# Kernel optimization log

Hardware: AMD Instinct MI355X
Metric: run time of the kernel (lower is better)

## Reference

```python
import jax, jax.numpy as jnp
import numpy as np

D_MODEL = 1024
EXPERT_SIZE = 512
N_EXPERTS = 8
GROUP_SIZE = 32
BATCH = 32
SEQ = 2048
TEMPERATURE = 1.0


def setup_inputs() -> dict:
    key = jax.random.key(0)
    k_x, k_l1, k_l2, k_c = jax.random.split(key, 4)
    x = jax.random.normal(k_x, (BATCH, SEQ, D_MODEL), dtype=jnp.float32)
    # truncated-normal-style init approximated with normal scaled by 1/sqrt(fan_in)
    lin1 = jax.random.normal(k_l1, (N_EXPERTS, D_MODEL, EXPERT_SIZE), dtype=jnp.float32) * (D_MODEL ** -0.5)
    lin2 = jax.random.normal(k_l2, (N_EXPERTS, EXPERT_SIZE, D_MODEL), dtype=jnp.float32) * (EXPERT_SIZE ** -0.5)
    controller = jax.random.normal(k_c, (D_MODEL, N_EXPERTS), dtype=jnp.float32) * (D_MODEL ** -0.5)
    return {"x": x, "lin1": lin1, "lin2": lin2, "controller": controller}


def reference(x, lin1, lin2, controller):
    B, S, D = x.shape
    # group_tokens: sparsity_dim=0 -> transpose to (S, B, D), split batch into groups
    xg = jnp.transpose(x, (1, 0, 2)).reshape(S, B // GROUP_SIZE, GROUP_SIZE, D)  # (s, g, k, d)
    # controller logits, softmax over the group (token) axis k (dim=-2)
    logits = jnp.einsum("sgkd,de->sgke", xg, controller) / TEMPERATURE
    merge_w = jax.nn.softmax(logits, axis=-2)  # (s, g, k, e)
    emit_w = merge_w  # default: emit softmax over tokens, same temp -> reuse
    # merge: weighted sum of tokens per expert
    merged = jnp.einsum("sgke,sgkd->sged", merge_w, xg)  # (s, g, e, d)
    # per-expert MLP
    h = jax.nn.relu(jnp.einsum("sged,edf->sgef", merged, lin1))  # (s, g, e, f)
    expert_out = jnp.einsum("sgef,efd->sged", h, lin2)  # (s, g, e, d)
    # emit back to tokens
    out = jnp.einsum("sgke,sged->sgkd", emit_w, expert_out)  # (s, g, k, d)
    # redistribute: (S, B, D) -> (B, S, D)
    return jnp.transpose(out.reshape(S, B, D), (1, 0, 2))
```

## Files before the change

### kernel.cpp

```cpp
#include <hip/hip_runtime.h>
#include <hip/hip_bf16.h>

#define SS 2048
#define BB 32
#define DD 1024
#define FF 512
#define EE 8

typedef __attribute__((ext_vector_type(8))) short short8;
typedef __attribute__((ext_vector_type(8))) unsigned short ushort8v;
typedef __attribute__((ext_vector_type(4))) unsigned short ushort4v;
typedef __attribute__((ext_vector_type(4))) float f32x4;

__device__ inline unsigned short f2bf(float f) {
  union { float f; unsigned u; } v; v.f = f;
  return (unsigned short)((v.u + 0x7FFFu + ((v.u >> 16) & 1u)) >> 16);
}
__device__ inline float bf2f(unsigned short h) {
  union { unsigned u; float f; } v; v.u = ((unsigned)h) << 16;
  return v.f;
}

__global__ __launch_bounds__(256) void transpose_bf16(
    const float* __restrict__ in, unsigned short* __restrict__ out, int K, int N) {
  __shared__ float tile[32][33];
  int e = blockIdx.z;
  const float* inp = in + (size_t)e * K * N;
  unsigned short* outp = out + (size_t)e * K * N;
  int k0 = blockIdx.x * 32, n0 = blockIdx.y * 32;
  int tx = threadIdx.x;
  int ty = threadIdx.y;
#pragma unroll
  for (int i = 0; i < 4; i++) {
    int k = ty + i * 8;
    tile[k][tx] = inp[(size_t)(k0 + k) * N + n0 + tx];
  }
  __syncthreads();
#pragma unroll
  for (int i = 0; i < 4; i++) {
    int n = ty + i * 8;
    outp[(size_t)(n0 + n) * K + k0 + tx] = f2bf(tile[tx][n]);
  }
}

__global__ __launch_bounds__(256) void logits_k(
    const float* __restrict__ x,
    const float* __restrict__ ctrl,
    float* __restrict__ lgT) {
  int t = threadIdx.x;
  __shared__ __align__(16) float cs[EE * DD];
  for (int i = t; i < DD * EE; i += 256) {
    int d = i >> 3, e = i & 7;
    cs[e * DD + (d ^ (((d >> 6) & 7) << 2))] = ctrl[i];
  }
  __syncthreads();

  int g = t >> 4, c = t & 15;
  int m0 = blockIdx.x * 64 + g * 4;
  const float* xr = x + (size_t)m0 * DD;
  float acc[4][8] = {};
#pragma unroll 4
  for (int i = 0; i < 16; i++) {
    int db = c * 4 + i * 64;
    float4 c4[8];
#pragma unroll
    for (int e = 0; e < 8; e++)
      c4[e] = *(const float4*)&cs[e * DD + i * 64 + ((c ^ (i & 7)) << 2)];
#pragma unroll
    for (int r = 0; r < 4; r++) {
      float4 xv = *(const float4*)&xr[(size_t)r * DD + db];
#pragma unroll
      for (int e = 0; e < 8; e++)
        acc[r][e] += xv.x * c4[e].x + xv.y * c4[e].y + xv.z * c4[e].z + xv.w * c4[e].w;
    }
  }
#pragma unroll
  for (int off = 1; off < 16; off <<= 1)
#pragma unroll
    for (int r = 0; r < 4; r++)
#pragma unroll
      for (int e = 0; e < 8; e++)
        acc[r][e] += __shfl_xor(acc[r][e], off, 64);
  if (c == 0) {
#pragma unroll
    for (int r = 0; r < 4; r++) {
      int m = m0 + r;
      int s = m & (SS - 1), k = m >> 11;
      float* p = &lgT[((size_t)s * BB + k) * EE];
      float4 lo = {acc[r][0], acc[r][1], acc[r][2], acc[r][3]};
      float4 hi = {acc[r][4], acc[r][5], acc[r][6], acc[r][7]};
      *(float4*)p = lo;
      *(float4*)(p + 4) = hi;
    }
  }
}

__global__ __launch_bounds__(256) void softmax_k(
    const float* __restrict__ lgT,
    float* __restrict__ mw) {
  int t = threadIdx.x;
  int sl = t >> 5, k = t & 31;
  size_t s = (size_t)blockIdx.x * 8 + sl;
  const float* p = &lgT[(s * BB + k) * EE];
  float v[8];
  float4 lo = *(const float4*)p, hi = *(const float4*)(p + 4);
  v[0]=lo.x; v[1]=lo.y; v[2]=lo.z; v[3]=lo.w; v[4]=hi.x; v[5]=hi.y; v[6]=hi.z; v[7]=hi.w;
  float mx[8];
#pragma unroll
  for (int e = 0; e < 8; e++) mx[e] = v[e];
#pragma unroll
  for (int off = 1; off < 32; off <<= 1)
#pragma unroll
    for (int e = 0; e < 8; e++)
      mx[e] = fmaxf(mx[e], __shfl_xor(mx[e], off, 64));
  float pr[8], sm[8];
#pragma unroll
  for (int e = 0; e < 8; e++) { pr[e] = __expf(v[e] - mx[e]); sm[e] = pr[e]; }
#pragma unroll
  for (int off = 1; off < 32; off <<= 1)
#pragma unroll
    for (int e = 0; e < 8; e++)
      sm[e] += __shfl_xor(sm[e], off, 64);
  float4 o0 = {pr[0]/sm[0], pr[1]/sm[1], pr[2]/sm[2], pr[3]/sm[3]};
  float4 o1 = {pr[4]/sm[4], pr[5]/sm[5], pr[6]/sm[6], pr[7]/sm[7]};
  float* q = &mw[(s * BB + k) * EE];
  *(float4*)q = o0;
  *(float4*)(q + 4) = o1;
}

__global__ __launch_bounds__(256) void merge_v(
    const float* __restrict__ x,
    const float* __restrict__ mw,
    unsigned short* __restrict__ merged) {
  int s = blockIdx.x;
  int t = threadIdx.x;
  __shared__ __align__(16) float wl[BB][EE];
  wl[t >> 3][t & 7] = mw[(size_t)s * BB * EE + t];
  __syncthreads();
  int d0 = t * 4;
  float a[8][4] = {};
#pragma unroll 4
  for (int k = 0; k < 32; k++) {
    float4 xv = *(const float4*)&x[((size_t)k * SS + s) * DD + d0];
    float4 wA = *(const float4*)&wl[k][0];
    float4 wB = *(const float4*)&wl[k][4];
    a[0][0] += wA.x * xv.x; a[0][1] += wA.x * xv.y; a[0][2] += wA.x * xv.z; a[0][3] += wA.x * xv.w;
    a[1][0] += wA.y * xv.x; a[1][1] += wA.y * xv.y; a[1][2] += wA.y * xv.z; a[1][3] += wA.y * xv.w;
    a[2][0] += wA.z * xv.x; a[2][1] += wA.z * xv.y; a[2][2] += wA.z * xv.z; a[2][3] += wA.z * xv.w;
    a[3][0] += wA.w * xv.x; a[3][1] += wA.w * xv.y; a[3][2] += wA.w * xv.z; a[3][3] += wA.w * xv.w;
    a[4][0] += wB.x * xv.x; a[4][1] += wB.x * xv.y; a[4][2] += wB.x * xv.z; a[4][3] += wB.x * xv.w;
    a[5][0] += wB.y * xv.x; a[5][1] += wB.y * xv.y; a[5][2] += wB.y * xv.z; a[5][3] += wB.y * xv.w;
    a[6][0] += wB.z * xv.x; a[6][1] += wB.z * xv.y; a[6][2] += wB.z * xv.z; a[6][3] += wB.z * xv.w;
    a[7][0] += wB.w * xv.x; a[7][1] += wB.w * xv.y; a[7][2] += wB.w * xv.z; a[7][3] += wB.w * xv.w;
  }
#pragma unroll
  for (int e = 0; e < 8; e++) {
    ushort4v pv;
    pv[0] = f2bf(a[e][0]); pv[1] = f2bf(a[e][1]);
    pv[2] = f2bf(a[e][2]); pv[3] = f2bf(a[e][3]);
    *(ushort4v*)&merged[((size_t)e * SS + s) * DD + d0] = pv;
  }
}

template <int RELU>
__global__ __launch_bounds__(256) void gemm_bt(
    const unsigned short* __restrict__ A, const unsigned short* __restrict__ Bt,
    unsigned short* __restrict__ C, int K, int N) {
  int e = blockIdx.z;
  int m0 = blockIdx.x * 128;
  int n0 = blockIdx.y * 128;
  const unsigned short* Ae = A + (size_t)e * SS * K;
  const unsigned short* Be = Bt + (size_t)e * N * K;
  unsigned short* Ce = C + (size_t)e * SS * N;

  __shared__ __align__(16) unsigned short As[128 * 32];
  __shared__ __align__(16) unsigned short Bs[128 * 32];

  int t = threadIdx.x;
  int lane = t & 63, w = t >> 6;
  int wm = w >> 1, wn = w & 1;
  int lr = lane & 15;
  int kh = lane >> 4;
  int khs = kh ^ ((lr >> 1) & 3);

  f32x4 acc[4][4] = {};

  for (int kt = 0; kt < K; kt += 32) {
#pragma unroll
    for (int i = 0; i < 2; i++) {
      int c = t + i * 256;
      int r = c >> 2;
      int subg = (c & 3) ^ ((r >> 1) & 3);
      __builtin_amdgcn_global_load_lds(
          (const __attribute__((address_space(1))) void*)(Ae + (size_t)(m0 + r) * K + kt + subg * 8),
          (__attribute__((address_space(3))) void*)(&As[c * 8]), 16, 0, 0);
      __builtin_amdgcn_global_load_lds(
          (const __attribute__((address_space(1))) void*)(Be + (size_t)(n0 + r) * K + kt + subg * 8),
          (__attribute__((address_space(3))) void*)(&Bs[c * 8]), 16, 0, 0);
    }
    __syncthreads();

    short8 af[4], bfr[4];
#pragma unroll
    for (int mi = 0; mi < 4; mi++)
      af[mi] = *(const short8*)&As[(wm * 64 + mi * 16 + lr) * 32 + khs * 8];
#pragma unroll
    for (int ni = 0; ni < 4; ni++)
      bfr[ni] = *(const short8*)&Bs[(wn * 64 + ni * 16 + lr) * 32 + khs * 8];
#pragma unroll
    for (int mi = 0; mi < 4; mi++)
#pragma unroll
      for (int ni = 0; ni < 4; ni++)
        acc[mi][ni] = __builtin_amdgcn_mfma_f32_16x16x32_bf16(af[mi], bfr[ni], acc[mi][ni], 0, 0, 0);
    __syncthreads();
  }

  int rb = (lane >> 4) * 4;
  int cb = lane & 15;
#pragma unroll
  for (int mi = 0; mi < 4; mi++)
#pragma unroll
    for (int ni = 0; ni < 4; ni++)
#pragma unroll
      for (int r = 0; r < 4; r++) {
        float v = acc[mi][ni][r];
        if (RELU) v = fmaxf(v, 0.f);
        int m = m0 + wm * 64 + mi * 16 + rb + r;
        int n = n0 + wn * 64 + ni * 16 + cb;
        Ce[(size_t)m * N + n] = f2bf(v);
      }
}

__global__ __launch_bounds__(256) void emit_out(
    const unsigned short* __restrict__ eo,
    const float* __restrict__ mw,
    float* __restrict__ out) {
  int s = blockIdx.x;
  int t = threadIdx.x;
  __shared__ float wsm[BB][EE];
  wsm[t >> 3][t & 7] = mw[(size_t)s * BB * EE + t];
  __syncthreads();
  int d0 = t * 4;
  float ev[EE][4];
#pragma unroll
  for (int e2 = 0; e2 < 8; e2++) {
    ushort4v v = *(const ushort4v*)&eo[((size_t)e2 * SS + s) * DD + d0];
    ev[e2][0] = bf2f(v[0]); ev[e2][1] = bf2f(v[1]);
    ev[e2][2] = bf2f(v[2]); ev[e2][3] = bf2f(v[3]);
  }
  for (int b = 0; b < BB; b++) {
    float o0 = 0.f, o1 = 0.f, o2 = 0.f, o3 = 0.f;
#pragma unroll
    for (int e2 = 0; e2 < 8; e2++) {
      float we = wsm[b][e2];
      o0 += we * ev[e2][0]; o1 += we * ev[e2][1];
      o2 += we * ev[e2][2]; o3 += we * ev[e2][3];
    }
    float4 ov = {o0, o1, o2, o3};
    *(float4*)&out[((size_t)b * SS + s) * DD + d0] = ov;
  }
}

extern "C" void kernel_launch(void* const* d_in, const int* in_sizes, int n_in,
                              void* d_out, int out_size, void* d_ws, size_t ws_size,
                              hipStream_t stream) {
  const float* x = (const float*)d_in[0];
  const float* lin1 = (const float*)d_in[1];
  const float* lin2 = (const float*)d_in[2];
  const float* ctrl = (const float*)d_in[3];
  float* out = (float*)d_out;

  char* ws = (char*)d_ws;
  size_t off = 0;
  unsigned short* lin1t = (unsigned short*)(ws + off); off += (size_t)EE * DD * FF * 2;
  unsigned short* lin2t = (unsigned short*)(ws + off); off += (size_t)EE * FF * DD * 2;
  unsigned short* merged = (unsigned short*)(ws + off); off += (size_t)SS * EE * DD * 2;
  unsigned short* hbuf = (unsigned short*)(ws + off); off += (size_t)SS * EE * FF * 2;
  unsigned short* eo = (unsigned short*)(ws + off); off += (size_t)SS * EE * DD * 2;
  float* mw = (float*)(ws + off); off += (size_t)SS * BB * EE * 4;
  float* lgT = (float*)(ws + off); off += (size_t)SS * BB * EE * 4;

  dim3 tb(32, 8);
  transpose_bf16<<<dim3(DD / 32, FF / 32, EE), tb, 0, stream>>>(lin1, lin1t, DD, FF);
  transpose_bf16<<<dim3(FF / 32, DD / 32, EE), tb, 0, stream>>>(lin2, lin2t, FF, DD);

  logits_k<<<(SS * BB) / 64, 256, 0, stream>>>(x, ctrl, lgT);
  softmax_k<<<SS / 8, 256, 0, stream>>>(lgT, mw);
  merge_v<<<SS, 256, 0, stream>>>(x, mw, merged);

  gemm_bt<1><<<dim3(SS / 128, FF / 128, EE), 256, 0, stream>>>(merged, lin1t, hbuf, DD, FF);
  gemm_bt<0><<<dim3(SS / 128, DD / 128, EE), 256, 0, stream>>>(hbuf, lin2t, eo, FF, DD);

  emit_out<<<SS, 256, 0, stream>>>(eo, mw, out);
}
```

Before: 340.6 us.

## Double-buffer LDS tiles in expert GEMM to overlap global loads with MFMA

The expert GEMM kernel now keeps two LDS buffers for the A and B tiles. It issues the async global-to-LDS loads for the next K-step before computing on the current one, with explicit vmcnt waits and barriers in place of __syncthreads. This is meant to hide global memory latency behind the MFMA work. It doubles LDS use per block, which may lower occupancy, and it relies on hand-placed waitcnt values being correct.

```diff
diff --git a/kernel.cpp b/kernel.cpp
--- a/kernel.cpp
+++ b/kernel.cpp
@@ -173,8 +173,8 @@
   const unsigned short* Be = Bt + (size_t)e * N * K;
   unsigned short* Ce = C + (size_t)e * SS * N;
 
-  __shared__ __align__(16) unsigned short As[128 * 32];
-  __shared__ __align__(16) unsigned short Bs[128 * 32];
+  __shared__ __align__(16) unsigned short As[2][128 * 32];
+  __shared__ __align__(16) unsigned short Bs[2][128 * 32];
 
   int t = threadIdx.x;
   int lane = t & 63, w = t >> 6;
@@ -183,37 +183,61 @@
   int kh = lane >> 4;
   int khs = kh ^ ((lr >> 1) & 3);
 
+  int c0 = t, c1 = t + 256;
+  int r0 = c0 >> 2, r1 = c1 >> 2;
+  int sg0 = (c0 & 3) ^ ((r0 >> 1) & 3);
+  int sg1 = (c1 & 3) ^ ((r1 >> 1) & 3);
+
+#define STAGE(buf, kt)                                                                        \
+  do {                                                                                        \
+    __builtin_amdgcn_global_load_lds(                                                         \
+        (const __attribute__((address_space(1))) void*)(Ae + (size_t)(m0 + r0) * K + (kt) + sg0 * 8), \
+        (__attribute__((address_space(3))) void*)(&As[buf][c0 * 8]), 16, 0, 0);               \
+    __builtin_amdgcn_global_load_lds(                                                         \
+        (const __attribute__((address_space(1))) void*)(Be + (size_t)(n0 + r0) * K + (kt) + sg0 * 8), \
+        (__attribute__((address_space(3))) void*)(&Bs[buf][c0 * 8]), 16, 0, 0);               \
+    __builtin_amdgcn_global_load_lds(                                                         \
+        (const __attribute__((address_space(1))) void*)(Ae + (size_t)(m0 + r1) * K + (kt) + sg1 * 8), \
+        (__attribute__((address_space(3))) void*)(&As[buf][c1 * 8]), 16, 0, 0);               \
+    __builtin_amdgcn_global_load_lds(                                                         \
+        (const __attribute__((address_space(1))) void*)(Be + (size_t)(n0 + r1) * K + (kt) + sg1 * 8), \
+        (__attribute__((address_space(3))) void*)(&Bs[buf][c1 * 8]), 16, 0, 0);               \
+  } while (0)
+
   f32x4 acc[4][4] = {};
-
-  for (int kt = 0; kt < K; kt += 32) {
-#pragma unroll
-    for (int i = 0; i < 2; i++) {
-      int c = t + i * 256;
-      int r = c >> 2;
-      int subg = (c & 3) ^ ((r >> 1) & 3);
-      __builtin_amdgcn_global_load_lds(
-          (const __attribute__((address_space(1))) void*)(Ae + (size_t)(m0 + r) * K + kt + subg * 8),
-          (__attribute__((address_space(3))) void*)(&As[c * 8]), 16, 0, 0);
-      __builtin_amdgcn_global_load_lds(
-          (const __attribute__((address_space(1))) void*)(Be + (size_t)(n0 + r) * K + kt + subg * 8),
-          (__attribute__((address_space(3))) void*)(&Bs[c * 8]), 16, 0, 0);
+  int nk = K / 32;
+
+  STAGE(0, 0);
+
+  for (int s = 0; s < nk; ++s) {
+    int cur = s & 1;
+    if (s + 1 < nk) {
+      STAGE(cur ^ 1, (s + 1) * 32);
+      asm volatile("s_waitcnt vmcnt(4)" ::: "memory");
+    } else {
+      asm volatile("s_waitcnt vmcnt(0)" ::: "memory");
     }
-    __syncthreads();
+    __builtin_amdgcn_sched_barrier(0);
+    __builtin_amdgcn_s_barrier();
 
     short8 af[4], bfr[4];
 #pragma unroll
     for (int mi = 0; mi < 4; mi++)
-      af[mi] = *(const short8*)&As[(wm * 64 + mi * 16 + lr) * 32 + khs * 8];
+      af[mi] = *(const short8*)&As[cur][(wm * 64 + mi * 16 + lr) * 32 + khs * 8];
 #pragma unroll
     for (int ni = 0; ni < 4; ni++)
-      bfr[ni] = *(const short8*)&Bs[(wn * 64 + ni * 16 + lr) * 32 + khs * 8];
+      bfr[ni] = *(const short8*)&Bs[cur][(wn * 64 + ni * 16 + lr) * 32 + khs * 8];
 #pragma unroll
     for (int mi = 0; mi < 4; mi++)
 #pragma unroll
       for (int ni = 0; ni < 4; ni++)
         acc[mi][ni] = __builtin_amdgcn_mfma_f32_16x16x32_bf16(af[mi], bfr[ni], acc[mi][ni], 0, 0, 0);
-    __syncthreads();
-  }
+
+    asm volatile("s_waitcnt lgkmcnt(0)" ::: "memory");
+    __builtin_amdgcn_sched_barrier(0);
+    __builtin_amdgcn_s_barrier();
+  }
+#undef STAGE
 
   int rb = (lane >> 4) * 4;
   int cb = lane & 15;
```

New measurement: 337.4 us. No clear change (-0.9%).
